# Kernel tuning notes

Hardware: AMD Instinct MI355X
Metric: run time of the kernel (lower is better)

Reference implementation:

```python
import jax, jax.numpy as jnp
import numpy as np

EPS = 1e-5

def _conv1x1(x, w, b):
    # x: [B,C,...], w: [O,C], b: [O]
    y = jnp.einsum('oc,bc...->bo...', w, x)
    return y + b.reshape((1, -1) + (1,) * (x.ndim - 2))

def _bn(x, g, be, m, v):
    # inference-mode BatchNorm with running stats (PyTorch eps=1e-5)
    s = (1, -1) + (1,) * (x.ndim - 2)
    return (x - m.reshape(s)) * (g.reshape(s) / jnp.sqrt(v.reshape(s) + EPS)) + be.reshape(s)

def _patches3x3(x):
    # F.unfold(kernel=3, pad=1, stride=1, dil=1): [B,C,H,W] -> [B,C,9,H,W], row-major kernel order
    B, C, H, W = x.shape
    xp = jnp.pad(x, ((0, 0), (0, 0), (1, 1), (1, 1)))
    return jnp.stack([xp[:, :, ky:ky + H, kx:kx + W] for ky in range(3) for kx in range(3)], axis=2)

def setup_inputs() -> dict:
    key = jax.random.key(0)
    ks = jax.random.split(key, 40)
    B, Cin, H, W = 4, 16, 192, 192
    Cm = 64  # mlp[-1]
    d = {}
    d['x'] = jax.random.normal(ks[0], (B, Cin, H, W), jnp.float32)
    d['group_mask'] = jnp.ones((B, 1, H, W), jnp.float32)
    d['group_xyz'] = jax.random.normal(ks[1], (B, 3, 9, H, W), jnp.float32)
    def bnp(k, c):
        k1, k2, k3, k4 = jax.random.split(k, 4)
        return (1.0 + 0.1 * jax.random.normal(k1, (c,)), 0.1 * jax.random.normal(k2, (c,)),
                0.1 * jax.random.normal(k3, (c,)), 0.5 + jax.random.uniform(k4, (c,)))
    d['w0'] = 0.1 * jax.random.normal(ks[2], (Cm, Cin)); d['b0'] = 0.01 * jax.random.normal(ks[3], (Cm,))
    d['g0'], d['beta0'], d['m0'], d['v0'] = bnp(ks[4], Cm)
    wn_dims = [(8, 3), (8, 8), (16, 8)]
    for i, (o, c) in enumerate(wn_dims):
        d[f'wn_w{i}'] = 0.3 * jax.random.normal(ks[5 + 3 * i], (o, c))
        d[f'wn_b{i}'] = 0.01 * jax.random.normal(ks[6 + 3 * i], (o,))
        d[f'wn_g{i}'], d[f'wn_beta{i}'], d[f'wn_m{i}'], d[f'wn_v{i}'] = bnp(ks[7 + 3 * i], o)
    d['lw'] = 0.05 * jax.random.normal(ks[20], (Cm, 16 * Cm)); d['lb'] = 0.01 * jax.random.normal(ks[21], (Cm,))
    d['lg'], d['lbeta'], d['lm'], d['lv'] = bnp(ks[22], Cm)
    return d

def reference(x, group_mask, group_xyz,
              w0, b0, g0, beta0, m0, v0,
              wn_w0, wn_b0, wn_g0, wn_beta0, wn_m0, wn_v0,
              wn_w1, wn_b1, wn_g1, wn_beta1, wn_m1, wn_v1,
              wn_w2, wn_b2, wn_g2, wn_beta2, wn_m2, wn_v2,
              lw, lb, lg, lbeta, lm, lv):
    # mlp_convs chain (single layer here)
    x = jax.nn.relu(_bn(_conv1x1(x, w0, b0), g0, beta0, m0, v0))  # [B,Cm,H,W]
    B, _, N, H, W = group_xyz.shape
    # WeightNet on local coords: [B,3,N,H*W] -> [B,16,N,H*W]
    gz = group_xyz.reshape(B, 3, N, H * W)
    for w, b, g, be, m, v in ((wn_w0, wn_b0, wn_g0, wn_beta0, wn_m0, wn_v0),
                              (wn_w1, wn_b1, wn_g1, wn_beta1, wn_m1, wn_v1),
                              (wn_w2, wn_b2, wn_g2, wn_beta2, wn_m2, wn_v2)):
        gz = jax.nn.relu(_bn(_conv1x1(gz, w, b), g, be, m, v))
    gz = gz.reshape(B, 16, N, H, W)
    p = _patches3x3(x)  # [B,Cm,9,H,W]
    C = p.shape[1]
    # per-pixel matmul: [B,H,W,C,9] @ [B,H,W,9,16] -> [B,H,W,C,16]
    out = jnp.einsum('bckhw,bokhw->bhwco', p, gz)
    out = out.reshape(B, H, W, C * 16).transpose(0, 3, 1, 2)  # [B,16*Cm,H,W]
    return jax.nn.relu(_bn(_conv1x1(out, lw, lb), lg, lbeta, lm, lv))
```

## Files before the change

kernel.cpp:

```cpp
#include <hip/hip_runtime.h>
#include <hip/hip_bf16.h>

#define HH 192
#define WW 192
#define HWPROD (192*192)
#define EPSBN 1e-5f

typedef _Float16 f16x8 __attribute__((ext_vector_type(8)));
typedef _Float16 f16x4 __attribute__((ext_vector_type(4)));
typedef _Float16 f16x2 __attribute__((ext_vector_type(2)));
typedef float f32x4 __attribute__((ext_vector_type(4)));
typedef float f32x16 __attribute__((ext_vector_type(16)));

__global__ __launch_bounds__(256) void prep_conv0_k(
                       const float* __restrict__ w0, const float* __restrict__ b0,
                       const float* __restrict__ g0, const float* __restrict__ beta0,
                       const float* __restrict__ m0, const float* __restrict__ v0,
                       const float* __restrict__ wnw0, const float* __restrict__ wnb0,
                       const float* __restrict__ wng0, const float* __restrict__ wnbe0,
                       const float* __restrict__ wnm0, const float* __restrict__ wnv0,
                       const float* __restrict__ wnw1, const float* __restrict__ wnb1,
                       const float* __restrict__ wng1, const float* __restrict__ wnbe1,
                       const float* __restrict__ wnm1, const float* __restrict__ wnv1,
                       const float* __restrict__ wnw2, const float* __restrict__ wnb2,
                       const float* __restrict__ wng2, const float* __restrict__ wnbe2,
                       const float* __restrict__ wnm2, const float* __restrict__ wnv2,
                       const float* __restrict__ lw, const float* __restrict__ lb,
                       const float* __restrict__ lg, const float* __restrict__ lbeta,
                       const float* __restrict__ lm, const float* __restrict__ lv,
                       const float* __restrict__ x,
                       _Float16* __restrict__ x1L,
                       _Float16* __restrict__ whF,
                       float* __restrict__ lbf,
                       float* __restrict__ wnP)
{
    const int tid = threadIdx.x;

    if (blockIdx.x >= 1152) {
        int idx = (blockIdx.x - 1152) * 256 + tid;
        if (idx < 65536) {
            int j    = idx & 7;
            int lane = (idx >> 3) & 63;
            int kg   = (idx >> 9) & 63;
            int nt   = idx >> 15;
            int k = kg * 16 + ((lane >> 5) & 1) * 8 + j;
            int n = nt * 32 + (lane & 31);
            float s = lg[n] * rsqrtf(lv[n] + EPSBN);
            whF[idx] = (_Float16)(lw[n * 1024 + k] * s);
        } else if (idx < 65600) {
            int j = idx - 65536;
            float s = lg[j] * rsqrtf(lv[j] + EPSBN);
            lbf[j] = (lb[j] - lm[j]) * s + lbeta[j];
        } else if (idx < 65848) {
            int t = idx - 65600;
            if (t < 24)       { int o = t / 3;           float s = wng0[o] * rsqrtf(wnv0[o] + EPSBN); wnP[t] = wnw0[t] * s; }
            else if (t < 32)  { int o = t - 24;          float s = wng0[o] * rsqrtf(wnv0[o] + EPSBN); wnP[t] = (wnb0[o] - wnm0[o]) * s + wnbe0[o]; }
            else if (t < 96)  { int t2 = t - 32;  int o = t2 >> 3; float s = wng1[o] * rsqrtf(wnv1[o] + EPSBN); wnP[t] = wnw1[t2] * s; }
            else if (t < 104) { int o = t - 96;          float s = wng1[o] * rsqrtf(wnv1[o] + EPSBN); wnP[t] = (wnb1[o] - wnm1[o]) * s + wnbe1[o]; }
            else if (t < 232) { int t2 = t - 104; int o = t2 >> 3; float s = wng2[o] * rsqrtf(wnv2[o] + EPSBN); wnP[t] = wnw2[t2] * s; }
            else if (t < 248) { int o = t - 232;         float s = wng2[o] * rsqrtf(wnv2[o] + EPSBN); wnP[t] = (wnb2[o] - wnm2[o]) * s + wnbe2[o]; }
        }
        return;
    }

    __shared__ float wSt[16][64];
    __shared__ float bS[64];
    for (int t = tid; t < 1024; t += 256) {
        int o = t >> 4, ci = t & 15;
        float s = g0[o] * rsqrtf(v0[o] + EPSBN);
        wSt[ci][o] = w0[t] * s;
    }
    if (tid < 64) {
        float s = g0[tid] * rsqrtf(v0[tid] + EPSBN);
        bS[tid] = (b0[tid] - m0[tid]) * s + beta0[tid];
    }
    __syncthreads();

    const int pixb = blockIdx.x * 128;
    const int b  = pixb / HWPROD;
    const int pb = pixb - b * HWPROD;
    const int p4  = tid >> 3;
    const int oct = tid & 7;

    float xv[4][16];
#pragma unroll
    for (int q = 0; q < 4; q++) {
        const int p = pb + q * 32 + p4;
#pragma unroll
        for (int cin = 0; cin < 16; cin++)
            xv[q][cin] = x[((size_t)b * 16 + cin) * HWPROD + p];
    }

    const f32x4* wSt4 = reinterpret_cast<const f32x4*>(wSt);
    const f32x4* bS4  = reinterpret_cast<const f32x4*>(bS);

    f32x4 acc[4][2];
    {
        f32x4 ba = bS4[oct * 2], bb = bS4[oct * 2 + 1];
#pragma unroll
        for (int q = 0; q < 4; q++) { acc[q][0] = ba; acc[q][1] = bb; }
    }
#pragma unroll
    for (int cin = 0; cin < 16; cin++) {
        const f32x4 wa = wSt4[cin * 16 + oct * 2];
        const f32x4 wb = wSt4[cin * 16 + oct * 2 + 1];
#pragma unroll
        for (int q = 0; q < 4; q++) {
            const float xc = xv[q][cin];
            const f32x4 xb = { xc, xc, xc, xc };
            acc[q][0] = __builtin_elementwise_fma(xb, wa, acc[q][0]);
            acc[q][1] = __builtin_elementwise_fma(xb, wb, acc[q][1]);
        }
    }
    const f32x4 z4 = { 0.f, 0.f, 0.f, 0.f };
#pragma unroll
    for (int q = 0; q < 4; q++) {
        union { f16x4 h4[2]; f16x8 v; } O;
        O.h4[0] = __builtin_convertvector(__builtin_elementwise_max(acc[q][0], z4), f16x4);
        O.h4[1] = __builtin_convertvector(__builtin_elementwise_max(acc[q][1], z4), f16x4);
        *(f16x8*)(x1L + (size_t)(pixb + q * 32 + p4) * 64 + oct * 8) = O.v;
    }
}

__global__ __launch_bounds__(128, 2) void pconv_main_k(const float* __restrict__ gxyz,
                                                       const _Float16* __restrict__ x1L,
                                                       const _Float16* __restrict__ whF,
                                                       const float* __restrict__ lbf,
                                                       const float* __restrict__ wnP,
                                                       float* __restrict__ out)
{
    __shared__ __align__(16) char smem[19456];
    unsigned*  xSu = reinterpret_cast<unsigned*>(smem);
    _Float16*  gzF = reinterpret_cast<_Float16*>(smem);
    float*     Cb  = reinterpret_cast<float*>(smem);

    const int tid = threadIdx.x;
    const int bid = blockIdx.x;
    const int b   = bid / (96 * 6);
    const int rem = bid % (96 * 6);
    const int hb  = rem / 6;
    const int c6  = rem % 6;
    const int h   = hb * 2;
    const int wc0 = c6 * 32;

    for (int u = tid; u < 576; u += 128) {
        int col = u & 31, rrow = (u >> 5) & 1, tap = u >> 6;
        size_t base = ((size_t)(b * 3) * 9 + tap) * HWPROD + (size_t)(h + rrow) * WW + wc0 + col;
        float z0 = gxyz[base];
        float z1 = gxyz[base + (size_t)9 * HWPROD];
        float z2 = gxyz[base + (size_t)18 * HWPROD];
        float h0[8], h1[8];
#pragma unroll
        for (int o = 0; o < 8; o++) {
            float a = wnP[24 + o] + wnP[o * 3 + 0] * z0 + wnP[o * 3 + 1] * z1 + wnP[o * 3 + 2] * z2;
            h0[o] = fmaxf(a, 0.f);
        }
#pragma unroll
        for (int o = 0; o < 8; o++) {
            float a = wnP[96 + o];
#pragma unroll
            for (int c = 0; c < 8; c++) a += wnP[32 + o * 8 + c] * h0[c];
            h1[o] = fmaxf(a, 0.f);
        }
        float g[16];
#pragma unroll
        for (int o = 0; o < 16; o++) {
            float a = wnP[232 + o];
#pragma unroll
            for (int c = 0; c < 8; c++) a += wnP[104 + o * 8 + c] * h1[c];
            g[o] = fmaxf(a, 0.f);
        }
        f16x8 lo, hi;
#pragma unroll
        for (int o = 0; o < 8; o++) { lo[o] = (_Float16)g[o]; hi[o] = (_Float16)g[o + 8]; }
        int pixb = u & 63;
        *(f16x8*)&gzF[pixb * 152 + tap * 16]     = lo;
        *(f16x8*)&gzF[pixb * 152 + tap * 16 + 8] = hi;
    }
    __syncthreads();

    const int lane = tid & 63;
    const int w    = tid >> 6;
    const int p31  = lane & 31;
    const int oh   = lane >> 5;
    const int pixb = w * 32 + p31;

    f16x2 gq2[9][4];
#pragma unroll
    for (int t = 0; t < 9; t++) {
        union { f16x8 v; f16x2 h[4]; } G;
        G.v = *(const f16x8*)&gzF[pixb * 152 + t * 16 + oh * 8];
#pragma unroll
        for (int d = 0; d < 4; d++) gq2[t][d] = G.h[d];
    }
    __syncthreads();

    for (int i = 0; i < 16; i++) {
        int u  = i * 128 + tid;
        int cq = u & 15;
        int cc = ((u >> 4) & 31) + 1;
        int rr = u >> 9;
        int hr = h + rr - 1;
        uint2 v = {0u, 0u};
        if (hr >= 0 && hr < HH)
            v = *(const uint2*)(x1L + (((size_t)b * HH + hr) * WW + wc0 + cc - 1) * 64 + cq * 4);
        xSu[(2 * cq) * 137 + rr * 34 + cc]     = v.x;
        xSu[(2 * cq + 1) * 137 + rr * 34 + cc] = v.y;
    }
    {
        int cq   = tid & 15;
        int side = (tid >> 4) & 1;
        int rr   = tid >> 5;
        int cc   = side ? 33 : 0;
        int hr = h + rr - 1;
        int wc = wc0 + cc - 1;
        uint2 v = {0u, 0u};
        if (hr >= 0 && hr < HH && wc >= 0 && wc < WW)
            v = *(const uint2*)(x1L + (((size_t)b * HH + hr) * WW + wc) * 64 + cq * 4);
        xSu[(2 * cq) * 137 + rr * 34 + cc]     = v.x;
        xSu[(2 * cq + 1) * 137 + rr * 34 + cc] = v.y;
    }
    __syncthreads();

    const f16x8* whF8 = (const f16x8*)whF;
    const unsigned* xrow = xSu + w * 34 + p31;

    f32x16 facc0, facc1;
#pragma unroll
    for (int r = 0; r < 16; r++) { facc0[r] = 0.f; facc1[r] = 0.f; }

#pragma unroll 2
    for (int cb = 0; cb < 32; cb++) {
        const int c0 = 2 * cb, c1 = 2 * cb + 1;
        const f16x8 wh00 = whF8[(0 * 64 + c0) * 64 + lane];
        const f16x8 wh01 = whF8[(1 * 64 + c0) * 64 + lane];
        const f16x8 wh10 = whF8[(0 * 64 + c1) * 64 + lane];
        const f16x8 wh11 = whF8[(1 * 64 + c1) * 64 + lane];

        union { f16x2 h2[4]; f16x8 v; } av0, av1;
#pragma unroll
        for (int d = 0; d < 4; d++) { av0.h2[d] = f16x2{0, 0}; av1.h2[d] = f16x2{0, 0}; }
        const unsigned* xr = xrow + cb * 137;
#pragma unroll
        for (int ky = 0; ky < 3; ky++) {
#pragma unroll
            for (int kx = 0; kx < 3; kx++) {
                const int t = ky * 3 + kx;
                f16x2 xq;
                { unsigned tmp = xr[ky * 34 + kx]; xq = *(f16x2*)&tmp; }
#pragma unroll
                for (int d = 0; d < 4; d++) {
                    asm("v_pk_fma_f16 %0, %1, %2, %0 op_sel:[0,0,0] op_sel_hi:[0,1,1]"
                        : "+v"(av0.h2[d]) : "v"(xq), "v"(gq2[t][d]));
                    asm("v_pk_fma_f16 %0, %1, %2, %0 op_sel:[1,0,0] op_sel_hi:[1,1,1]"
                        : "+v"(av1.h2[d]) : "v"(xq), "v"(gq2[t][d]));
                }
            }
        }
        facc0 = __builtin_amdgcn_mfma_f32_32x32x16_f16(av0.v, wh00, facc0, 0, 0, 0);
        facc1 = __builtin_amdgcn_mfma_f32_32x32x16_f16(av0.v, wh01, facc1, 0, 0, 0);
        facc0 = __builtin_amdgcn_mfma_f32_32x32x16_f16(av1.v, wh10, facc0, 0, 0, 0);
        facc1 = __builtin_amdgcn_mfma_f32_32x32x16_f16(av1.v, wh11, facc1, 0, 0, 0);
    }
    __syncthreads();

    {
        const int n0 = p31;
        const float bias0 = lbf[n0];
        const float bias1 = lbf[n0 + 32];
#pragma unroll
        for (int r = 0; r < 16; r++) {
            const int m = (r & 3) + 8 * (r >> 2) + 4 * oh;
            Cb[n0 * 67 + w * 32 + m]        = fmaxf(facc0[r] + bias0, 0.f);
            Cb[(n0 + 32) * 67 + w * 32 + m] = fmaxf(facc1[r] + bias1, 0.f);
        }
    }
    __syncthreads();
    {
        const int col = tid & 31;
        const int nq  = tid >> 5;
#pragma unroll
        for (int rr = 0; rr < 2; rr++) {
            size_t ob = ((size_t)b * 64 + nq * 16) * HWPROD + (size_t)(h + rr) * WW + wc0 + col;
#pragma unroll
            for (int i = 0; i < 16; i++)
                out[ob + (size_t)i * HWPROD] = Cb[(nq * 16 + i) * 67 + rr * 32 + col];
        }
    }
}

extern "C" void kernel_launch(void* const* d_in, const int* in_sizes, int n_in,
                              void* d_out, int out_size, void* d_ws, size_t ws_size,
                              hipStream_t stream) {
    const float* x    = (const float*)d_in[0];
    const float* gxyz = (const float*)d_in[2];

    char* ws = (char*)d_ws;
    _Float16* x1L = (_Float16*)ws;
    _Float16* whF = x1L + 9437184;
    float* lbf = (float*)(whF + 65536);
    float* wnP = lbf + 64;

    prep_conv0_k<<<1414, 256, 0, stream>>>(
        (const float*)d_in[3],  (const float*)d_in[4],  (const float*)d_in[5],
        (const float*)d_in[6],  (const float*)d_in[7],  (const float*)d_in[8],
        (const float*)d_in[9],  (const float*)d_in[10], (const float*)d_in[11],
        (const float*)d_in[12], (const float*)d_in[13], (const float*)d_in[14],
        (const float*)d_in[15], (const float*)d_in[16], (const float*)d_in[17],
        (const float*)d_in[18], (const float*)d_in[19], (const float*)d_in[20],
        (const float*)d_in[21], (const float*)d_in[22], (const float*)d_in[23],
        (const float*)d_in[24], (const float*)d_in[25], (const float*)d_in[26],
        (const float*)d_in[27], (const float*)d_in[28], (const float*)d_in[29],
        (const float*)d_in[30], (const float*)d_in[31], (const float*)d_in[32],
        x, x1L, whF, lbf, wnP);

    pconv_main_k<<<4 * 96 * 6, 128, 0, stream>>>(gxyz, x1L, whF, lbf, wnP,
                                                 (float*)d_out);
}
```

Measured before the change: 214.1 us.

## Convert main kernel to persistent blocks pulling strips via atomic counter

The main kernel now launches a fixed 2048 blocks that loop, each taking the next strip index from a global atomic counter until all 2304 strips are processed. The prep kernel resets the counter. The aim is to cut the tail-wave imbalance and block launch overhead of the fixed 2304-block grid. In exchange it adds one atomic and one barrier per strip, and the loop needs extra barriers so shared memory is not overwritten while still in use.

```diff
diff --git a/kernel.cpp b/kernel.cpp
--- a/kernel.cpp
+++ b/kernel.cpp
@@ -5,6 +5,7 @@
 #define WW 192
 #define HWPROD (192*192)
 #define EPSBN 1e-5f
+#define NSTRIP 2304
 
 typedef _Float16 f16x8 __attribute__((ext_vector_type(8)));
 typedef _Float16 f16x4 __attribute__((ext_vector_type(4)));
@@ -32,7 +33,8 @@
                        _Float16* __restrict__ x1L,
                        _Float16* __restrict__ whF,
                        float* __restrict__ lbf,
-                       float* __restrict__ wnP)
+                       float* __restrict__ wnP,
+                       int* __restrict__ cnt)
 {
     const int tid = threadIdx.x;
 
@@ -59,6 +61,8 @@
             else if (t < 104) { int o = t - 96;          float s = wng1[o] * rsqrtf(wnv1[o] + EPSBN); wnP[t] = (wnb1[o] - wnm1[o]) * s + wnbe1[o]; }
             else if (t < 232) { int t2 = t - 104; int o = t2 >> 3; float s = wng2[o] * rsqrtf(wnv2[o] + EPSBN); wnP[t] = wnw2[t2] * s; }
             else if (t < 248) { int o = t - 232;         float s = wng2[o] * rsqrtf(wnv2[o] + EPSBN); wnP[t] = (wnb2[o] - wnm2[o]) * s + wnbe2[o]; }
+        } else if (idx == 65848) {
+            *cnt = 0;
         }
         return;
     }
@@ -127,164 +131,171 @@
                                                        const _Float16* __restrict__ whF,
                                                        const float* __restrict__ lbf,
                                                        const float* __restrict__ wnP,
+                                                       int* cnt,
                                                        float* __restrict__ out)
 {
     __shared__ __align__(16) char smem[19456];
+    __shared__ int sW;
     unsigned*  xSu = reinterpret_cast<unsigned*>(smem);
     _Float16*  gzF = reinterpret_cast<_Float16*>(smem);
     float*     Cb  = reinterpret_cast<float*>(smem);
 
     const int tid = threadIdx.x;
-    const int bid = blockIdx.x;
-    const int b   = bid / (96 * 6);
-    const int rem = bid % (96 * 6);
-    const int hb  = rem / 6;
-    const int c6  = rem % 6;
-    const int h   = hb * 2;
-    const int wc0 = c6 * 32;
-
-    for (int u = tid; u < 576; u += 128) {
-        int col = u & 31, rrow = (u >> 5) & 1, tap = u >> 6;
-        size_t base = ((size_t)(b * 3) * 9 + tap) * HWPROD + (size_t)(h + rrow) * WW + wc0 + col;
-        float z0 = gxyz[base];
-        float z1 = gxyz[base + (size_t)9 * HWPROD];
-        float z2 = gxyz[base + (size_t)18 * HWPROD];
-        float h0[8], h1[8];
-#pragma unroll
-        for (int o = 0; o < 8; o++) {
-            float a = wnP[24 + o] + wnP[o * 3 + 0] * z0 + wnP[o * 3 + 1] * z1 + wnP[o * 3 + 2] * z2;
-            h0[o] = fmaxf(a, 0.f);
-        }
-#pragma unroll
-        for (int o = 0; o < 8; o++) {
-            float a = wnP[96 + o];
-#pragma unroll
-            for (int c = 0; c < 8; c++) a += wnP[32 + o * 8 + c] * h0[c];
-            h1[o] = fmaxf(a, 0.f);
-        }
-        float g[16];
-#pragma unroll
-        for (int o = 0; o < 16; o++) {
-            float a = wnP[232 + o];
-#pragma unroll
-            for (int c = 0; c < 8; c++) a += wnP[104 + o * 8 + c] * h1[c];
-            g[o] = fmaxf(a, 0.f);
-        }
-        f16x8 lo, hi;
-#pragma unroll
-        for (int o = 0; o < 8; o++) { lo[o] = (_Float16)g[o]; hi[o] = (_Float16)g[o + 8]; }
-        int pixb = u & 63;
-        *(f16x8*)&gzF[pixb * 152 + tap * 16]     = lo;
-        *(f16x8*)&gzF[pixb * 152 + tap * 16 + 8] = hi;
-    }
-    __syncthreads();
-
     const int lane = tid & 63;
     const int w    = tid >> 6;
     const int p31  = lane & 31;
     const int oh   = lane >> 5;
     const int pixb = w * 32 + p31;
-
-    f16x2 gq2[9][4];
-#pragma unroll
-    for (int t = 0; t < 9; t++) {
-        union { f16x8 v; f16x2 h[4]; } G;
-        G.v = *(const f16x8*)&gzF[pixb * 152 + t * 16 + oh * 8];
-#pragma unroll
-        for (int d = 0; d < 4; d++) gq2[t][d] = G.h[d];
-    }
-    __syncthreads();
-
-    for (int i = 0; i < 16; i++) {
-        int u  = i * 128 + tid;
-        int cq = u & 15;
-        int cc = ((u >> 4) & 31) + 1;
-        int rr = u >> 9;
-        int hr = h + rr - 1;
-        uint2 v = {0u, 0u};
-        if (hr >= 0 && hr < HH)
-            v = *(const uint2*)(x1L + (((size_t)b * HH + hr) * WW + wc0 + cc - 1) * 64 + cq * 4);
-        xSu[(2 * cq) * 137 + rr * 34 + cc]     = v.x;
-        xSu[(2 * cq + 1) * 137 + rr * 34 + cc] = v.y;
-    }
-    {
-        int cq   = tid & 15;
-        int side = (tid >> 4) & 1;
-        int rr   = tid >> 5;
-        int cc   = side ? 33 : 0;
-        int hr = h + rr - 1;
-        int wc = wc0 + cc - 1;
-        uint2 v = {0u, 0u};
-        if (hr >= 0 && hr < HH && wc >= 0 && wc < WW)
-            v = *(const uint2*)(x1L + (((size_t)b * HH + hr) * WW + wc) * 64 + cq * 4);
-        xSu[(2 * cq) * 137 + rr * 34 + cc]     = v.x;
-        xSu[(2 * cq + 1) * 137 + rr * 34 + cc] = v.y;
-    }
-    __syncthreads();
-
     const f16x8* whF8 = (const f16x8*)whF;
     const unsigned* xrow = xSu + w * 34 + p31;
 
-    f32x16 facc0, facc1;
-#pragma unroll
-    for (int r = 0; r < 16; r++) { facc0[r] = 0.f; facc1[r] = 0.f; }
+    while (true) {
+        if (tid == 0) sW = atomicAdd(cnt, 1);
+        __syncthreads();
+        const int s = sW;
+        if (s >= NSTRIP) break;
+
+        const int b   = s / (96 * 6);
+        const int rem = s % (96 * 6);
+        const int hb  = rem / 6;
+        const int c6  = rem % 6;
+        const int h   = hb * 2;
+        const int wc0 = c6 * 32;
+
+        for (int u = tid; u < 576; u += 128) {
+            int col = u & 31, rrow = (u >> 5) & 1, tap = u >> 6;
+            size_t base = ((size_t)(b * 3) * 9 + tap) * HWPROD + (size_t)(h + rrow) * WW + wc0 + col;
+            float z0 = gxyz[base];
+            float z1 = gxyz[base + (size_t)9 * HWPROD];
+            float z2 = gxyz[base + (size_t)18 * HWPROD];
+            float h0[8], h1[8];
+#pragma unroll
+            for (int o = 0; o < 8; o++) {
+                float a = wnP[24 + o] + wnP[o * 3 + 0] * z0 + wnP[o * 3 + 1] * z1 + wnP[o * 3 + 2] * z2;
+                h0[o] = fmaxf(a, 0.f);
+            }
+#pragma unroll
+            for (int o = 0; o < 8; o++) {
+                float a = wnP[96 + o];
+#pragma unroll
+                for (int c = 0; c < 8; c++) a += wnP[32 + o * 8 + c] * h0[c];
+                h1[o] = fmaxf(a, 0.f);
+            }
+            float g[16];
+#pragma unroll
+            for (int o = 0; o < 16; o++) {
+                float a = wnP[232 + o];
+#pragma unroll
+                for (int c = 0; c < 8; c++) a += wnP[104 + o * 8 + c] * h1[c];
+                g[o] = fmaxf(a, 0.f);
+            }
+            f16x8 lo, hi;
+#pragma unroll
+            for (int o = 0; o < 8; o++) { lo[o] = (_Float16)g[o]; hi[o] = (_Float16)g[o + 8]; }
+            int px = u & 63;
+            *(f16x8*)&gzF[px * 152 + tap * 16]     = lo;
+            *(f16x8*)&gzF[px * 152 + tap * 16 + 8] = hi;
+        }
+        __syncthreads();
+
+        f16x2 gq2[9][4];
+#pragma unroll
+        for (int t = 0; t < 9; t++) {
+            union { f16x8 v; f16x2 h[4]; } G;
+            G.v = *(const f16x8*)&gzF[pixb * 152 + t * 16 + oh * 8];
+#pragma unroll
+            for (int d = 0; d < 4; d++) gq2[t][d] = G.h[d];
+        }
+        __syncthreads();
+
+        for (int i = 0; i < 16; i++) {
+            int u  = i * 128 + tid;
+            int cq = u & 15;
+            int cc = ((u >> 4) & 31) + 1;
+            int rr = u >> 9;
+            int hr = h + rr - 1;
+            uint2 v = {0u, 0u};
+            if (hr >= 0 && hr < HH)
+                v = *(const uint2*)(x1L + (((size_t)b * HH + hr) * WW + wc0 + cc - 1) * 64 + cq * 4);
+            xSu[(2 * cq) * 137 + rr * 34 + cc]     = v.x;
+            xSu[(2 * cq + 1) * 137 + rr * 34 + cc] = v.y;
+        }
+        {
+            int cq   = tid & 15;
+            int side = (tid >> 4) & 1;
+            int rr   = tid >> 5;
+            int cc   = side ? 33 : 0;
+            int hr = h + rr - 1;
+            int wc = wc0 + cc - 1;
+            uint2 v = {0u, 0u};
+            if (hr >= 0 && hr < HH && wc >= 0 && wc < WW)
+                v = *(const uint2*)(x1L + (((size_t)b * HH + hr) * WW + wc) * 64 + cq * 4);
+            xSu[(2 * cq) * 137 + rr * 34 + cc]     = v.x;
+            xSu[(2 * cq + 1) * 137 + rr * 34 + cc] = v.y;
+        }
+        __syncthreads();
+
+        f32x16 facc0, facc1;
+#pragma unroll
+        for (int r = 0; r < 16; r++) { facc0[r] = 0.f; facc1[r] = 0.f; }
 
 #pragma unroll 2
-    for (int cb = 0; cb < 32; cb++) {
-        const int c0 = 2 * cb, c1 = 2 * cb + 1;
-        const f16x8 wh00 = whF8[(0 * 64 + c0) * 64 + lane];
-        const f16x8 wh01 = whF8[(1 * 64 + c0) * 64 + lane];
-        const f16x8 wh10 = whF8[(0 * 64 + c1) * 64 + lane];
-        const f16x8 wh11 = whF8[(1 * 64 + c1) * 64 + lane];
-
-        union { f16x2 h2[4]; f16x8 v; } av0, av1;
-#pragma unroll
-        for (int d = 0; d < 4; d++) { av0.h2[d] = f16x2{0, 0}; av1.h2[d] = f16x2{0, 0}; }
-        const unsigned* xr = xrow + cb * 137;
-#pragma unroll
-        for (int ky = 0; ky < 3; ky++) {
-#pragma unroll
-            for (int kx = 0; kx < 3; kx++) {
-                const int t = ky * 3 + kx;
-                f16x2 xq;
-                { unsigned tmp = xr[ky * 34 + kx]; xq = *(f16x2*)&tmp; }
-#pragma unroll
-                for (int d = 0; d < 4; d++) {
-                    asm("v_pk_fma_f16 %0, %1, %2, %0 op_sel:[0,0,0] op_sel_hi:[0,1,1]"
-                        : "+v"(av0.h2[d]) : "v"(xq), "v"(gq2[t][d]));
-                    asm("v_pk_fma_f16 %0, %1, %2, %0 op_sel:[1,0,0] op_sel_hi:[1,1,1]"
-                        : "+v"(av1.h2[d]) : "v"(xq), "v"(gq2[t][d]));
+        for (int cb = 0; cb < 32; cb++) {
+            const int c0 = 2 * cb, c1 = 2 * cb + 1;
+            const f16x8 wh00 = whF8[(0 * 64 + c0) * 64 + lane];
+            const f16x8 wh01 = whF8[(1 * 64 + c0) * 64 + lane];
+            const f16x8 wh10 = whF8[(0 * 64 + c1) * 64 + lane];
+            const f16x8 wh11 = whF8[(1 * 64 + c1) * 64 + lane];
+
+            union { f16x2 h2[4]; f16x8 v; } av0, av1;
+#pragma unroll
+            for (int d = 0; d < 4; d++) { av0.h2[d] = f16x2{0, 0}; av1.h2[d] = f16x2{0, 0}; }
+            const unsigned* xr = xrow + cb * 137;
+#pragma unroll
+            for (int ky = 0; ky < 3; ky++) {
+#pragma unroll
+                for (int kx = 0; kx < 3; kx++) {
+                    const int t = ky * 3 + kx;
+                    f16x2 xq;
+                    { unsigned tmp = xr[ky * 34 + kx]; xq = *(f16x2*)&tmp; }
+#pragma unroll
+                    for (int d = 0; d < 4; d++) {
+                        asm("v_pk_fma_f16 %0, %1, %2, %0 op_sel:[0,0,0] op_sel_hi:[0,1,1]"
+                            : "+v"(av0.h2[d]) : "v"(xq), "v"(gq2[t][d]));
+                        asm("v_pk_fma_f16 %0, %1, %2, %0 op_sel:[1,0,0] op_sel_hi:[1,1,1]"
+                            : "+v"(av1.h2[d]) : "v"(xq), "v"(gq2[t][d]));
+                    }
                 }
             }
-        }
-        facc0 = __builtin_amdgcn_mfma_f32_32x32x16_f16(av0.v, wh00, facc0, 0, 0, 0);
-        facc1 = __builtin_amdgcn_mfma_f32_32x32x16_f16(av0.v, wh01, facc1, 0, 0, 0);
-        facc0 = __builtin_amdgcn_mfma_f32_32x32x16_f16(av1.v, wh10, facc0, 0, 0, 0);
-        facc1 = __builtin_amdgcn_mfma_f32_32x32x16_f16(av1.v, wh11, facc1, 0, 0, 0);
-    }
-    __syncthreads();
-
-    {
-        const int n0 = p31;
-        const float bias0 = lbf[n0];
-        const float bias1 = lbf[n0 + 32];
-#pragma unroll
-        for (int r = 0; r < 16; r++) {
-            const int m = (r & 3) + 8 * (r >> 2) + 4 * oh;
-            Cb[n0 * 67 + w * 32 + m]        = fmaxf(facc0[r] + bias0, 0.f);
-            Cb[(n0 + 32) * 67 + w * 32 + m] = fmaxf(facc1[r] + bias1, 0.f);
-        }
-    }
-    __syncthreads();
-    {
-        const int col = tid & 31;
-        const int nq  = tid >> 5;
-#pragma unroll
-        for (int rr = 0; rr < 2; rr++) {
-            size_t ob = ((size_t)b * 64 + nq * 16) * HWPROD + (size_t)(h + rr) * WW + wc0 + col;
-#pragma unroll
-            for (int i = 0; i < 16; i++)
-                out[ob + (size_t)i * HWPROD] = Cb[(nq * 16 + i) * 67 + rr * 32 + col];
+            facc0 = __builtin_amdgcn_mfma_f32_32x32x16_f16(av0.v, wh00, facc0, 0, 0, 0);
+            facc1 = __builtin_amdgcn_mfma_f32_32x32x16_f16(av0.v, wh01, facc1, 0, 0, 0);
+            facc0 = __builtin_amdgcn_mfma_f32_32x32x16_f16(av1.v, wh10, facc0, 0, 0, 0);
+            facc1 = __builtin_amdgcn_mfma_f32_32x32x16_f16(av1.v, wh11, facc1, 0, 0, 0);
+        }
+        __syncthreads();
+
+        {
+            const int n0 = p31;
+            const float bias0 = lbf[n0];
+            const float bias1 = lbf[n0 + 32];
+#pragma unroll
+            for (int r = 0; r < 16; r++) {
+                const int m = (r & 3) + 8 * (r >> 2) + 4 * oh;
+                Cb[n0 * 67 + w * 32 + m]        = fmaxf(facc0[r] + bias0, 0.f);
+                Cb[(n0 + 32) * 67 + w * 32 + m] = fmaxf(facc1[r] + bias1, 0.f);
+            }
+        }
+        __syncthreads();
+        {
+            const int col = tid & 31;
+            const int nq  = tid >> 5;
+#pragma unroll
+            for (int rr = 0; rr < 2; rr++) {
+                size_t ob = ((size_t)b * 64 + nq * 16) * HWPROD + (size_t)(h + rr) * WW + wc0 + col;
+#pragma unroll
+                for (int i = 0; i < 16; i++)
+                    out[ob + (size_t)i * HWPROD] = Cb[(nq * 16 + i) * 67 + rr * 32 + col];
+            }
         }
     }
 }
@@ -300,6 +311,7 @@
     _Float16* whF = x1L + 9437184;
     float* lbf = (float*)(whF + 65536);
     float* wnP = lbf + 64;
+    int* cnt = (int*)(wnP + 248);
 
     prep_conv0_k<<<1414, 256, 0, stream>>>(
         (const float*)d_in[3],  (const float*)d_in[4],  (const float*)d_in[5],
@@ -312,8 +324,8 @@
         (const float*)d_in[24], (const float*)d_in[25], (const float*)d_in[26],
         (const float*)d_in[27], (const float*)d_in[28], (const float*)d_in[29],
         (const float*)d_in[30], (const float*)d_in[31], (const float*)d_in[32],
-        x, x1L, whF, lbf, wnP);
-
-    pconv_main_k<<<4 * 96 * 6, 128, 0, stream>>>(gxyz, x1L, whF, lbf, wnP,
-                                                 (float*)d_out);
+        x, x1L, whF, lbf, wnP, cnt);
+
+    pconv_main_k<<<2048, 128, 0, stream>>>(gxyz, x1L, whF, lbf, wnP, cnt,
+                                           (float*)d_out);
 }
```

After: 235.5 us. 10.0% more time.

## Shrink LDS by staging x in channel halves and computing weights in registers

Applied to the files above, without the earlier changes.

The main kernel now computes the WeightNet outputs directly in each lane's registers (each lane handles its own pixel and its half of the output channels) rather than staging them through shared memory. It stages the x halo tile in two channel halves and stages the second half after the first half's MFMA loop. The epilogue writes the output transpose in two passes. Together these cut shared memory from about 19 KB to about 8.7 KB, which may allow more resident blocks per CU. The cost is extra barriers, serialized staging of the second half with no overlap, and WeightNet work that the two half-lanes of each pixel now partly repeat.

```diff
diff --git a/kernel.cpp b/kernel.cpp
--- a/kernel.cpp
+++ b/kernel.cpp
@@ -129,9 +129,8 @@
                                                        const float* __restrict__ wnP,
                                                        float* __restrict__ out)
 {
-    __shared__ __align__(16) char smem[19456];
+    __shared__ __align__(16) char smem[8768];
     unsigned*  xSu = reinterpret_cast<unsigned*>(smem);
-    _Float16*  gzF = reinterpret_cast<_Float16*>(smem);
     float*     Cb  = reinterpret_cast<float*>(smem);
 
     const int tid = threadIdx.x;
@@ -143,9 +142,46 @@
     const int h   = hb * 2;
     const int wc0 = c6 * 32;
 
-    for (int u = tid; u < 576; u += 128) {
-        int col = u & 31, rrow = (u >> 5) & 1, tap = u >> 6;
-        size_t base = ((size_t)(b * 3) * 9 + tap) * HWPROD + (size_t)(h + rrow) * WW + wc0 + col;
+    const int lane = tid & 63;
+    const int w    = tid >> 6;
+    const int p31  = lane & 31;
+    const int oh   = lane >> 5;
+
+    auto stageHalf = [&](int hf) {
+#pragma unroll
+        for (int i = 0; i < 8; i++) {
+            int u   = i * 128 + tid;
+            int cqL = u & 7;
+            int cc  = ((u >> 3) & 31) + 1;
+            int rr  = u >> 8;
+            int hr = h + rr - 1;
+            uint2 v = {0u, 0u};
+            if (hr >= 0 && hr < HH)
+                v = *(const uint2*)(x1L + (((size_t)b * HH + hr) * WW + wc0 + cc - 1) * 64 + (hf * 8 + cqL) * 4);
+            xSu[(2 * cqL) * 137 + rr * 34 + cc]     = v.x;
+            xSu[(2 * cqL + 1) * 137 + rr * 34 + cc] = v.y;
+        }
+        if (tid < 64) {
+            int cqL  = tid & 7;
+            int side = (tid >> 3) & 1;
+            int rr   = tid >> 4;
+            int cc   = side ? 33 : 0;
+            int hr = h + rr - 1;
+            int wc = wc0 + cc - 1;
+            uint2 v = {0u, 0u};
+            if (hr >= 0 && hr < HH && wc >= 0 && wc < WW)
+                v = *(const uint2*)(x1L + (((size_t)b * HH + hr) * WW + wc) * 64 + (hf * 8 + cqL) * 4);
+            xSu[(2 * cqL) * 137 + rr * 34 + cc]     = v.x;
+            xSu[(2 * cqL + 1) * 137 + rr * 34 + cc] = v.y;
+        }
+    };
+
+    stageHalf(0);
+
+    f16x2 gq2[9][4];
+#pragma unroll
+    for (int tap = 0; tap < 9; tap++) {
+        size_t base = ((size_t)(b * 3) * 9 + tap) * HWPROD + (size_t)(h + w) * WW + wc0 + p31;
         float z0 = gxyz[base];
         float z1 = gxyz[base + (size_t)9 * HWPROD];
         float z2 = gxyz[base + (size_t)18 * HWPROD];
@@ -162,63 +198,18 @@
             for (int c = 0; c < 8; c++) a += wnP[32 + o * 8 + c] * h0[c];
             h1[o] = fmaxf(a, 0.f);
         }
-        float g[16];
-#pragma unroll
-        for (int o = 0; o < 16; o++) {
+        float g[8];
+#pragma unroll
+        for (int j = 0; j < 8; j++) {
+            const int o = oh * 8 + j;
             float a = wnP[232 + o];
 #pragma unroll
             for (int c = 0; c < 8; c++) a += wnP[104 + o * 8 + c] * h1[c];
-            g[o] = fmaxf(a, 0.f);
-        }
-        f16x8 lo, hi;
-#pragma unroll
-        for (int o = 0; o < 8; o++) { lo[o] = (_Float16)g[o]; hi[o] = (_Float16)g[o + 8]; }
-        int pixb = u & 63;
-        *(f16x8*)&gzF[pixb * 152 + tap * 16]     = lo;
-        *(f16x8*)&gzF[pixb * 152 + tap * 16 + 8] = hi;
-    }
-    __syncthreads();
-
-    const int lane = tid & 63;
-    const int w    = tid >> 6;
-    const int p31  = lane & 31;
-    const int oh   = lane >> 5;
-    const int pixb = w * 32 + p31;
-
-    f16x2 gq2[9][4];
-#pragma unroll
-    for (int t = 0; t < 9; t++) {
-        union { f16x8 v; f16x2 h[4]; } G;
-        G.v = *(const f16x8*)&gzF[pixb * 152 + t * 16 + oh * 8];
-#pragma unroll
-        for (int d = 0; d < 4; d++) gq2[t][d] = G.h[d];
-    }
-    __syncthreads();
-
-    for (int i = 0; i < 16; i++) {
-        int u  = i * 128 + tid;
-        int cq = u & 15;
-        int cc = ((u >> 4) & 31) + 1;
-        int rr = u >> 9;
-        int hr = h + rr - 1;
-        uint2 v = {0u, 0u};
-        if (hr >= 0 && hr < HH)
-            v = *(const uint2*)(x1L + (((size_t)b * HH + hr) * WW + wc0 + cc - 1) * 64 + cq * 4);
-        xSu[(2 * cq) * 137 + rr * 34 + cc]     = v.x;
-        xSu[(2 * cq + 1) * 137 + rr * 34 + cc] = v.y;
-    }
-    {
-        int cq   = tid & 15;
-        int side = (tid >> 4) & 1;
-        int rr   = tid >> 5;
-        int cc   = side ? 33 : 0;
-        int hr = h + rr - 1;
-        int wc = wc0 + cc - 1;
-        uint2 v = {0u, 0u};
-        if (hr >= 0 && hr < HH && wc >= 0 && wc < WW)
-            v = *(const uint2*)(x1L + (((size_t)b * HH + hr) * WW + wc) * 64 + cq * 4);
-        xSu[(2 * cq) * 137 + rr * 34 + cc]     = v.x;
-        xSu[(2 * cq + 1) * 137 + rr * 34 + cc] = v.y;
+            g[j] = fmaxf(a, 0.f);
+        }
+#pragma unroll
+        for (int d = 0; d < 4; d++)
+            gq2[tap][d] = f16x2{ (_Float16)g[2 * d], (_Float16)g[2 * d + 1] };
     }
     __syncthreads();
 
@@ -229,63 +220,72 @@
 #pragma unroll
     for (int r = 0; r < 16; r++) { facc0[r] = 0.f; facc1[r] = 0.f; }
 
+#pragma unroll 1
+    for (int hf = 0; hf < 2; hf++) {
 #pragma unroll 2
-    for (int cb = 0; cb < 32; cb++) {
-        const int c0 = 2 * cb, c1 = 2 * cb + 1;
-        const f16x8 wh00 = whF8[(0 * 64 + c0) * 64 + lane];
-        const f16x8 wh01 = whF8[(1 * 64 + c0) * 64 + lane];
-        const f16x8 wh10 = whF8[(0 * 64 + c1) * 64 + lane];
-        const f16x8 wh11 = whF8[(1 * 64 + c1) * 64 + lane];
-
-        union { f16x2 h2[4]; f16x8 v; } av0, av1;
-#pragma unroll
-        for (int d = 0; d < 4; d++) { av0.h2[d] = f16x2{0, 0}; av1.h2[d] = f16x2{0, 0}; }
-        const unsigned* xr = xrow + cb * 137;
-#pragma unroll
-        for (int ky = 0; ky < 3; ky++) {
-#pragma unroll
-            for (int kx = 0; kx < 3; kx++) {
-                const int t = ky * 3 + kx;
-                f16x2 xq;
-                { unsigned tmp = xr[ky * 34 + kx]; xq = *(f16x2*)&tmp; }
-#pragma unroll
-                for (int d = 0; d < 4; d++) {
-                    asm("v_pk_fma_f16 %0, %1, %2, %0 op_sel:[0,0,0] op_sel_hi:[0,1,1]"
-                        : "+v"(av0.h2[d]) : "v"(xq), "v"(gq2[t][d]));
-                    asm("v_pk_fma_f16 %0, %1, %2, %0 op_sel:[1,0,0] op_sel_hi:[1,1,1]"
-                        : "+v"(av1.h2[d]) : "v"(xq), "v"(gq2[t][d]));
+        for (int cl = 0; cl < 16; cl++) {
+            const int c0 = 2 * (hf * 16 + cl), c1 = c0 + 1;
+            const f16x8 wh00 = whF8[(0 * 64 + c0) * 64 + lane];
+            const f16x8 wh01 = whF8[(1 * 64 + c0) * 64 + lane];
+            const f16x8 wh10 = whF8[(0 * 64 + c1) * 64 + lane];
+            const f16x8 wh11 = whF8[(1 * 64 + c1) * 64 + lane];
+
+            union { f16x2 h2[4]; f16x8 v; } av0, av1;
+#pragma unroll
+            for (int d = 0; d < 4; d++) { av0.h2[d] = f16x2{0, 0}; av1.h2[d] = f16x2{0, 0}; }
+            const unsigned* xr = xrow + cl * 137;
+#pragma unroll
+            for (int ky = 0; ky < 3; ky++) {
+#pragma unroll
+                for (int kx = 0; kx < 3; kx++) {
+                    const int t = ky * 3 + kx;
+                    f16x2 xq;
+                    { unsigned tmp = xr[ky * 34 + kx]; xq = *(f16x2*)&tmp; }
+#pragma unroll
+                    for (int d = 0; d < 4; d++) {
+                        asm("v_pk_fma_f16 %0, %1, %2, %0 op_sel:[0,0,0] op_sel_hi:[0,1,1]"
+                            : "+v"(av0.h2[d]) : "v"(xq), "v"(gq2[t][d]));
+                        asm("v_pk_fma_f16 %0, %1, %2, %0 op_sel:[1,0,0] op_sel_hi:[1,1,1]"
+                            : "+v"(av1.h2[d]) : "v"(xq), "v"(gq2[t][d]));
+                    }
                 }
             }
-        }
-        facc0 = __builtin_amdgcn_mfma_f32_32x32x16_f16(av0.v, wh00, facc0, 0, 0, 0);
-        facc1 = __builtin_amdgcn_mfma_f32_32x32x16_f16(av0.v, wh01, facc1, 0, 0, 0);
-        facc0 = __builtin_amdgcn_mfma_f32_32x32x16_f16(av1.v, wh10, facc0, 0, 0, 0);
-        facc1 = __builtin_amdgcn_mfma_f32_32x32x16_f16(av1.v, wh11, facc1, 0, 0, 0);
-    }
-    __syncthreads();
-
-    {
-        const int n0 = p31;
-        const float bias0 = lbf[n0];
-        const float bias1 = lbf[n0 + 32];
-#pragma unroll
-        for (int r = 0; r < 16; r++) {
-            const int m = (r & 3) + 8 * (r >> 2) + 4 * oh;
-            Cb[n0 * 67 + w * 32 + m]        = fmaxf(facc0[r] + bias0, 0.f);
-            Cb[(n0 + 32) * 67 + w * 32 + m] = fmaxf(facc1[r] + bias1, 0.f);
-        }
-    }
-    __syncthreads();
-    {
-        const int col = tid & 31;
-        const int nq  = tid >> 5;
-#pragma unroll
-        for (int rr = 0; rr < 2; rr++) {
-            size_t ob = ((size_t)b * 64 + nq * 16) * HWPROD + (size_t)(h + rr) * WW + wc0 + col;
-#pragma unroll
-            for (int i = 0; i < 16; i++)
-                out[ob + (size_t)i * HWPROD] = Cb[(nq * 16 + i) * 67 + rr * 32 + col];
-        }
+            facc0 = __builtin_amdgcn_mfma_f32_32x32x16_f16(av0.v, wh00, facc0, 0, 0, 0);
+            facc1 = __builtin_amdgcn_mfma_f32_32x32x16_f16(av0.v, wh01, facc1, 0, 0, 0);
+            facc0 = __builtin_amdgcn_mfma_f32_32x32x16_f16(av1.v, wh10, facc0, 0, 0, 0);
+            facc1 = __builtin_amdgcn_mfma_f32_32x32x16_f16(av1.v, wh11, facc1, 0, 0, 0);
+        }
+        __syncthreads();
+        if (hf == 0) {
+            stageHalf(1);
+            __syncthreads();
+        }
+    }
+
+#pragma unroll 1
+    for (int pass = 0; pass < 2; pass++) {
+        const f32x16& fa = pass ? facc1 : facc0;
+        {
+            const float bias = lbf[pass * 32 + p31];
+#pragma unroll
+            for (int r = 0; r < 16; r++) {
+                const int m = (r & 3) + 8 * (r >> 2) + 4 * oh;
+                Cb[p31 * 65 + w * 32 + m] = fmaxf(fa[r] + bias, 0.f);
+            }
+        }
+        __syncthreads();
+        {
+            const int col = tid & 31;
+            const int nh  = tid >> 5;
+#pragma unroll
+            for (int rr = 0; rr < 2; rr++) {
+                size_t ob = ((size_t)b * 64 + pass * 32 + nh * 8) * HWPROD + (size_t)(h + rr) * WW + wc0 + col;
+#pragma unroll
+                for (int i = 0; i < 8; i++)
+                    out[ob + (size_t)i * HWPROD] = Cb[(nh * 8 + i) * 65 + rr * 32 + col];
+            }
+        }
+        if (pass == 0) __syncthreads();
     }
 }
 
```

Measured after the change: 230.4 us. 1.08x slower.

## Move WeightNet computation into prep kernel and stream packed results

Applied to the files above, without the earlier changes.

The per-pixel WeightNet MLP on group_xyz moves out of the main pconv kernel into extra blocks of the prep kernel. Those blocks fold the BatchNorm into the weights in shared memory and write f16 results to a workspace buffer, laid out so the main kernel loads them coalesced straight into registers. This removes the MLP arithmetic, one LDS staging pass and two barriers from the main kernel and trims its shared memory. The cost is an extra global write and read of the gz tensor (about 10 MB each way) and a longer prep kernel.

```diff
diff --git a/kernel.cpp b/kernel.cpp
--- a/kernel.cpp
+++ b/kernel.cpp
@@ -5,6 +5,7 @@
 #define WW 192
 #define HWPROD (192*192)
 #define EPSBN 1e-5f
+#define NSTRIP 2304
 
 typedef _Float16 f16x8 __attribute__((ext_vector_type(8)));
 typedef _Float16 f16x4 __attribute__((ext_vector_type(4)));
@@ -29,12 +30,78 @@
                        const float* __restrict__ lg, const float* __restrict__ lbeta,
                        const float* __restrict__ lm, const float* __restrict__ lv,
                        const float* __restrict__ x,
+                       const float* __restrict__ gxyz,
                        _Float16* __restrict__ x1L,
                        _Float16* __restrict__ whF,
                        float* __restrict__ lbf,
-                       float* __restrict__ wnP)
+                       float* __restrict__ wnP,
+                       unsigned* __restrict__ gzW)
 {
     const int tid = threadIdx.x;
+
+    if (blockIdx.x >= 1414) {
+        __shared__ float wp[248];
+        for (int t = tid; t < 248; t += 256) {
+            float v;
+            if (t < 24)       { int o = t / 3;           float s = wng0[o] * rsqrtf(wnv0[o] + EPSBN); v = wnw0[t] * s; }
+            else if (t < 32)  { int o = t - 24;          float s = wng0[o] * rsqrtf(wnv0[o] + EPSBN); v = (wnb0[o] - wnm0[o]) * s + wnbe0[o]; }
+            else if (t < 96)  { int t2 = t - 32;  int o = t2 >> 3; float s = wng1[o] * rsqrtf(wnv1[o] + EPSBN); v = wnw1[t2] * s; }
+            else if (t < 104) { int o = t - 96;          float s = wng1[o] * rsqrtf(wnv1[o] + EPSBN); v = (wnb1[o] - wnm1[o]) * s + wnbe1[o]; }
+            else if (t < 232) { int t2 = t - 104; int o = t2 >> 3; float s = wng2[o] * rsqrtf(wnv2[o] + EPSBN); v = wnw2[t2] * s; }
+            else              { int o = t - 232;         float s = wng2[o] * rsqrtf(wnv2[o] + EPSBN); v = (wnb2[o] - wnm2[o]) * s + wnbe2[o]; }
+            wp[t] = v;
+        }
+        __syncthreads();
+
+        const int s   = (blockIdx.x - 1414) * 4 + (tid >> 6);
+        const int t64 = tid & 63;
+        const int w   = t64 >> 5;
+        const int p31 = t64 & 31;
+        const int b   = s / (96 * 6);
+        const int rem = s % (96 * 6);
+        const int hb  = rem / 6;
+        const int c6  = rem % 6;
+        const int row = hb * 2 + w;
+        const int col = c6 * 32 + p31;
+
+#pragma unroll
+        for (int tap = 0; tap < 9; tap++) {
+            size_t base = ((size_t)(b * 3) * 9 + tap) * HWPROD + (size_t)row * WW + col;
+            float z0 = gxyz[base];
+            float z1 = gxyz[base + (size_t)9 * HWPROD];
+            float z2 = gxyz[base + (size_t)18 * HWPROD];
+            float h0[8], h1[8];
+#pragma unroll
+            for (int o = 0; o < 8; o++) {
+                float a = wp[24 + o] + wp[o * 3 + 0] * z0 + wp[o * 3 + 1] * z1 + wp[o * 3 + 2] * z2;
+                h0[o] = fmaxf(a, 0.f);
+            }
+#pragma unroll
+            for (int o = 0; o < 8; o++) {
+                float a = wp[96 + o];
+#pragma unroll
+                for (int c = 0; c < 8; c++) a += wp[32 + o * 8 + c] * h0[c];
+                h1[o] = fmaxf(a, 0.f);
+            }
+            float g[16];
+#pragma unroll
+            for (int o = 0; o < 16; o++) {
+                float a = wp[232 + o];
+#pragma unroll
+                for (int c = 0; c < 8; c++) a += wp[104 + o * 8 + c] * h1[c];
+                g[o] = fmaxf(a, 0.f);
+            }
+            unsigned* dst = gzW + (size_t)(s * 36 + tap * 4) * 128;
+#pragma unroll
+            for (int d = 0; d < 4; d++) {
+                f16x2 lo = { (_Float16)g[2 * d],     (_Float16)g[2 * d + 1] };
+                f16x2 hi = { (_Float16)g[8 + 2 * d], (_Float16)g[8 + 2 * d + 1] };
+                dst[d * 128 + w * 64 + p31]      = *(unsigned*)&lo;
+                dst[d * 128 + w * 64 + 32 + p31] = *(unsigned*)&hi;
+            }
+        }
+        return;
+    }
 
     if (blockIdx.x >= 1152) {
         int idx = (blockIdx.x - 1152) * 256 + tid;
@@ -122,16 +189,14 @@
     }
 }
 
-__global__ __launch_bounds__(128, 2) void pconv_main_k(const float* __restrict__ gxyz,
+__global__ __launch_bounds__(128, 2) void pconv_main_k(const unsigned* __restrict__ gzW,
                                                        const _Float16* __restrict__ x1L,
                                                        const _Float16* __restrict__ whF,
                                                        const float* __restrict__ lbf,
-                                                       const float* __restrict__ wnP,
                                                        float* __restrict__ out)
 {
-    __shared__ __align__(16) char smem[19456];
+    __shared__ __align__(16) char smem[17536];
     unsigned*  xSu = reinterpret_cast<unsigned*>(smem);
-    _Float16*  gzF = reinterpret_cast<_Float16*>(smem);
     float*     Cb  = reinterpret_cast<float*>(smem);
 
     const int tid = threadIdx.x;
@@ -143,57 +208,22 @@
     const int h   = hb * 2;
     const int wc0 = c6 * 32;
 
-    for (int u = tid; u < 576; u += 128) {
-        int col = u & 31, rrow = (u >> 5) & 1, tap = u >> 6;
-        size_t base = ((size_t)(b * 3) * 9 + tap) * HWPROD + (size_t)(h + rrow) * WW + wc0 + col;
-        float z0 = gxyz[base];
-        float z1 = gxyz[base + (size_t)9 * HWPROD];
-        float z2 = gxyz[base + (size_t)18 * HWPROD];
-        float h0[8], h1[8];
-#pragma unroll
-        for (int o = 0; o < 8; o++) {
-            float a = wnP[24 + o] + wnP[o * 3 + 0] * z0 + wnP[o * 3 + 1] * z1 + wnP[o * 3 + 2] * z2;
-            h0[o] = fmaxf(a, 0.f);
-        }
-#pragma unroll
-        for (int o = 0; o < 8; o++) {
-            float a = wnP[96 + o];
-#pragma unroll
-            for (int c = 0; c < 8; c++) a += wnP[32 + o * 8 + c] * h0[c];
-            h1[o] = fmaxf(a, 0.f);
-        }
-        float g[16];
-#pragma unroll
-        for (int o = 0; o < 16; o++) {
-            float a = wnP[232 + o];
-#pragma unroll
-            for (int c = 0; c < 8; c++) a += wnP[104 + o * 8 + c] * h1[c];
-            g[o] = fmaxf(a, 0.f);
-        }
-        f16x8 lo, hi;
-#pragma unroll
-        for (int o = 0; o < 8; o++) { lo[o] = (_Float16)g[o]; hi[o] = (_Float16)g[o + 8]; }
-        int pixb = u & 63;
-        *(f16x8*)&gzF[pixb * 152 + tap * 16]     = lo;
-        *(f16x8*)&gzF[pixb * 152 + tap * 16 + 8] = hi;
-    }
-    __syncthreads();
-
     const int lane = tid & 63;
     const int w    = tid >> 6;
     const int p31  = lane & 31;
     const int oh   = lane >> 5;
-    const int pixb = w * 32 + p31;
 
     f16x2 gq2[9][4];
-#pragma unroll
-    for (int t = 0; t < 9; t++) {
-        union { f16x8 v; f16x2 h[4]; } G;
-        G.v = *(const f16x8*)&gzF[pixb * 152 + t * 16 + oh * 8];
-#pragma unroll
-        for (int d = 0; d < 4; d++) gq2[t][d] = G.h[d];
-    }
-    __syncthreads();
+    {
+        const unsigned* gp = gzW + (size_t)bid * 36 * 128 + tid;
+#pragma unroll
+        for (int t = 0; t < 9; t++)
+#pragma unroll
+            for (int d = 0; d < 4; d++) {
+                unsigned u = gp[(t * 4 + d) * 128];
+                gq2[t][d] = *(f16x2*)&u;
+            }
+    }
 
     for (int i = 0; i < 16; i++) {
         int u  = i * 128 + tid;
@@ -300,8 +330,9 @@
     _Float16* whF = x1L + 9437184;
     float* lbf = (float*)(whF + 65536);
     float* wnP = lbf + 64;
-
-    prep_conv0_k<<<1414, 256, 0, stream>>>(
+    unsigned* gzW = (unsigned*)(wnP + 248);
+
+    prep_conv0_k<<<1990, 256, 0, stream>>>(
         (const float*)d_in[3],  (const float*)d_in[4],  (const float*)d_in[5],
         (const float*)d_in[6],  (const float*)d_in[7],  (const float*)d_in[8],
         (const float*)d_in[9],  (const float*)d_in[10], (const float*)d_in[11],
@@ -312,8 +343,8 @@
         (const float*)d_in[24], (const float*)d_in[25], (const float*)d_in[26],
         (const float*)d_in[27], (const float*)d_in[28], (const float*)d_in[29],
         (const float*)d_in[30], (const float*)d_in[31], (const float*)d_in[32],
-        x, x1L, whF, lbf, wnP);
-
-    pconv_main_k<<<4 * 96 * 6, 128, 0, stream>>>(gxyz, x1L, whF, lbf, wnP,
+        x, gxyz, x1L, whF, lbf, wnP, gzW);
+
+    pconv_main_k<<<4 * 96 * 6, 128, 0, stream>>>(gzW, x1L, whF, lbf,
                                                  (float*)d_out);
 }
```

Result: slower. 300.7 us (+40.5%).
